# Kernel tuning notes

Hardware: AMD Instinct MI355X
Metric: run time of the kernel (lower is better)

The kernel has to match this reference:

```python
import jax, jax.numpy as jnp
import numpy as np

B, C, H, W = 2, 512, 48, 48
HEADS = 8
REDUCTION = 4
DPH = max(C // REDUCTION // HEADS, 1)   # 16
TOTAL = DPH * HEADS                      # 128
EPS_NORM = 1e-12
EPS_BN = 1e-5


def setup_inputs() -> dict:
    key = jax.random.key(0)
    ks = jax.random.split(key, 6)
    x = jax.random.normal(ks[0], (B, C, H, W), dtype=jnp.float32)
    # 1x1 convs stored as [out_ch, in_ch] matrices
    w_qkv = jax.random.normal(ks[1], (3 * TOTAL, C), dtype=jnp.float32) * (1.0 / np.sqrt(C))
    w_out = jax.random.normal(ks[2], (C, TOTAL), dtype=jnp.float32) * (1.0 / np.sqrt(TOTAL))
    temperature = jnp.ones((HEADS, 1, 1), dtype=jnp.float32)
    bn_gamma = jnp.ones((C,), dtype=jnp.float32)
    bn_beta = jnp.zeros((C,), dtype=jnp.float32)
    return {"x": x, "w_qkv": w_qkv, "temperature": temperature,
            "w_out": w_out, "bn_gamma": bn_gamma, "bn_beta": bn_beta}


def _l2norm(t):
    # F.normalize(t, dim=-1): t / max(||t||_2, eps)
    n = jnp.sqrt(jnp.sum(t * t, axis=-1, keepdims=True))
    return t / jnp.maximum(n, EPS_NORM)


def reference(x, w_qkv, temperature, w_out, bn_gamma, bn_beta):
    b, c, h, w = x.shape
    n = h * w
    # qkv 1x1 conv: [b, 3*TOTAL, h, w]
    qkv = jnp.einsum('bchw,oc->bohw', x, w_qkv)
    q, k, v = jnp.split(qkv, 3, axis=1)
    # [b, heads, dph, n] -> [b, heads, n, dph]
    def heads_tokens(t):
        return t.reshape(b, HEADS, DPH, n).transpose(0, 1, 3, 2)
    q = _l2norm(heads_tokens(q))
    k = _l2norm(heads_tokens(k))
    v = heads_tokens(v)
    # [b, heads, n, n]
    attn = jnp.einsum('bhnd,bhmd->bhnm', q, k) * temperature[None]
    attn = jax.nn.softmax(attn, axis=-1)
    out = jnp.einsum('bhnm,bhmd->bhnd', attn, v)          # [b, heads, n, dph]
    out = out.transpose(0, 1, 3, 2).reshape(b, TOTAL, h, w)
    # project_out: 1x1 conv then BatchNorm2d (training-mode batch stats)
    out = jnp.einsum('bthw,ct->bchw', out, w_out)
    mean = jnp.mean(out, axis=(0, 2, 3))
    var = jnp.mean((out - mean[None, :, None, None]) ** 2, axis=(0, 2, 3))
    out = (out - mean[None, :, None, None]) * jax.lax.rsqrt(var + EPS_BN)[None, :, None, None]
    out = out * bn_gamma[None, :, None, None] + bn_beta[None, :, None, None]
    return out
```

## Files before the change

kernel.cpp:

```cpp
#include <hip/hip_runtime.h>

#define NB 2
#define CC 512
#define NN 2304
#define NH 8
#define DD 16
#define TT 128
#define O3 384

typedef __attribute__((ext_vector_type(4))) float f32x4;
typedef __attribute__((ext_vector_type(8))) __bf16 bf16x8;
typedef __attribute__((ext_vector_type(4))) __bf16 bf16x4;
typedef __attribute__((ext_vector_type(4))) _Float16 f16x4;

__global__ __launch_bounds__(256) void k0_convert(
    const float* __restrict__ x, const float* __restrict__ wqkv,
    const float* __restrict__ wout,
    __bf16* __restrict__ xT, __bf16* __restrict__ wqb, __bf16* __restrict__ wob)
{
    int bid = blockIdx.x;
    int t = threadIdx.x;
    if (bid < 576) {
        __shared__ float tile[64][65];
        int b = bid / 288, rem = bid % 288;
        int nt = rem / 8, cb = rem % 8;
        int n0 = nt * 64, c0 = cb * 64;
        int tc = t >> 6, tn = t & 63;
#pragma unroll
        for (int i = 0; i < 16; i++) {
            int cl = i * 4 + tc;
            tile[cl][tn] = x[(size_t)(b * CC + c0 + cl) * NN + n0 + tn];
        }
        __syncthreads();
#pragma unroll
        for (int i = 0; i < 16; i++) {
            int nl = i * 4 + tc;
            xT[(size_t)(b * NN + n0 + nl) * CC + c0 + tn] = (__bf16)tile[tn][nl];
        }
    } else {
        int wid = bid - 576;
        int base = wid * 256 + t;
#pragma unroll
        for (int i = 0; i < 16; i++) {
            int j = base + i * 16384;
            if (j < O3 * CC) wqb[j] = (__bf16)wqkv[j];
            else             wob[j - O3 * CC] = (__bf16)wout[j - O3 * CC];
        }
    }
}

__global__ __launch_bounds__(256) void k1_qkv(
    const __bf16* __restrict__ xT, const __bf16* __restrict__ wqb,
    _Float16* __restrict__ Q, _Float16* __restrict__ K, _Float16* __restrict__ VT)
{
    int ob = blockIdx.x, nt = blockIdx.y, b = blockIdx.z;
    int lane = threadIdx.x & 63, wave = threadIdx.x >> 6;
    int quad = lane >> 4, col = lane & 15;
    int n0 = nt * 64 + wave * 16;
    int o0 = ob * 32;

    f32x4 acc[2];
    acc[0] = (f32x4){0.f, 0.f, 0.f, 0.f};
    acc[1] = (f32x4){0.f, 0.f, 0.f, 0.f};

    const __bf16* arow = xT + (size_t)(b * NN + n0 + col) * CC + quad * 8;
    const __bf16* brow0 = wqb + (size_t)(o0 + col) * CC + quad * 8;
    const __bf16* brow1 = brow0 + 16 * CC;

    bf16x8 a  = *(const bf16x8*)(arow);
    bf16x8 w0 = *(const bf16x8*)(brow0);
    bf16x8 w1 = *(const bf16x8*)(brow1);
#pragma unroll
    for (int ks = 0; ks < 16; ks++) {
        bf16x8 an, wn0, wn1;
        if (ks < 15) {
            an  = *(const bf16x8*)(arow + (ks + 1) * 32);
            wn0 = *(const bf16x8*)(brow0 + (ks + 1) * 32);
            wn1 = *(const bf16x8*)(brow1 + (ks + 1) * 32);
        }
        acc[0] = __builtin_amdgcn_mfma_f32_16x16x32_bf16(a, w0, acc[0], 0, 0, 0);
        acc[1] = __builtin_amdgcn_mfma_f32_16x16x32_bf16(a, w1, acc[1], 0, 0, 0);
        a = an; w0 = wn0; w1 = wn1;
    }

#pragma unroll
    for (int s = 0; s < 2; s++) {
        int oc = o0 + s * 16 + col;
        int d = oc & 15, h = (oc >> 4) & 7, kind = oc >> 7;
        f32x4 v = acc[s];
        if (kind < 2) {
            float ss0 = v[0] * v[0], ss1 = v[1] * v[1], ss2 = v[2] * v[2], ss3 = v[3] * v[3];
#pragma unroll
            for (int m = 1; m < 16; m <<= 1) {
                ss0 += __shfl_xor(ss0, m);
                ss1 += __shfl_xor(ss1, m);
                ss2 += __shfl_xor(ss2, m);
                ss3 += __shfl_xor(ss3, m);
            }
            v[0] *= 1.0f / fmaxf(sqrtf(ss0), 1e-12f);
            v[1] *= 1.0f / fmaxf(sqrtf(ss1), 1e-12f);
            v[2] *= 1.0f / fmaxf(sqrtf(ss2), 1e-12f);
            v[3] *= 1.0f / fmaxf(sqrtf(ss3), 1e-12f);
            _Float16* dst = (kind == 0 ? Q : K) + (size_t)(b * NH + h) * NN * DD;
#pragma unroll
            for (int r = 0; r < 4; r++) {
                int n = n0 + quad * 4 + r;
                dst[(size_t)n * DD + d] = (_Float16)v[r];
            }
        } else {
            f16x4 pk;
#pragma unroll
            for (int r = 0; r < 4; r++) pk[r] = (_Float16)v[r];
            int n = n0 + quad * 4;
            *(f16x4*)(VT + (size_t)((b * NH + h) * DD + d) * NN + n) = pk;
        }
    }
}

__global__ __launch_bounds__(256) void k2_attn(
    const _Float16* __restrict__ Q, const _Float16* __restrict__ K,
    const _Float16* __restrict__ VT, const float* __restrict__ temp,
    float* __restrict__ Opart, float* __restrict__ Lpart)
{
    int qt = blockIdx.x, bh = blockIdx.y, sp = blockIdx.z;
    int lane = threadIdx.x & 63, wave = threadIdx.x >> 6;
    int quad = lane >> 4, col = lane & 15;
    int kbase = sp * 288;
    int qbase = qt * 256 + wave * 64;

    const _Float16* Qb = Q + (size_t)bh * NN * DD;
    float tl2 = temp[bh & 7] * 1.4426950408889634f;

    f16x4 qf0 = *(const f16x4*)(Qb + (size_t)(qbase +  0 + col) * DD + quad * 4);
    f16x4 qf1 = *(const f16x4*)(Qb + (size_t)(qbase + 16 + col) * DD + quad * 4);
    f16x4 qf2 = *(const f16x4*)(Qb + (size_t)(qbase + 32 + col) * DD + quad * 4);
    f16x4 qf3 = *(const f16x4*)(Qb + (size_t)(qbase + 48 + col) * DD + quad * 4);

    f32x4 oa0 = {0.f,0.f,0.f,0.f}, oa1 = {0.f,0.f,0.f,0.f};
    f32x4 oa2 = {0.f,0.f,0.f,0.f}, oa3 = {0.f,0.f,0.f,0.f};
    float la0 = 0.f, la1 = 0.f, la2 = 0.f, la3 = 0.f;
    const f32x4 zc = {0.f,0.f,0.f,0.f};

    const _Float16* kp = K + (size_t)bh * NN * DD + (size_t)(kbase + col) * DD + quad * 4;
    const _Float16* vp = VT + (size_t)bh * DD * NN + (size_t)col * NN + kbase + quad * 4;

    f16x4 kfa = *(const f16x4*)(kp);
    f16x4 kfb = *(const f16x4*)(kp + 16 * DD);
    f16x4 vfa = *(const f16x4*)(vp);
    f16x4 vfb = *(const f16x4*)(vp + 16);

#define K2_CHUNK(KF, VF)                                                        \
    {                                                                           \
        f32x4 s0 = __builtin_amdgcn_mfma_f32_16x16x16f16(KF, qf0, zc, 0, 0, 0); \
        f32x4 s1 = __builtin_amdgcn_mfma_f32_16x16x16f16(KF, qf1, zc, 0, 0, 0); \
        f32x4 s2 = __builtin_amdgcn_mfma_f32_16x16x16f16(KF, qf2, zc, 0, 0, 0); \
        f32x4 s3 = __builtin_amdgcn_mfma_f32_16x16x16f16(KF, qf3, zc, 0, 0, 0); \
        f16x4 p0, p1, p2, p3;                                                   \
        _Pragma("unroll")                                                       \
        for (int r = 0; r < 4; ++r) {                                           \
            float e0 = __builtin_amdgcn_exp2f(tl2 * s0[r]);                     \
            float e1 = __builtin_amdgcn_exp2f(tl2 * s1[r]);                     \
            float e2 = __builtin_amdgcn_exp2f(tl2 * s2[r]);                     \
            float e3 = __builtin_amdgcn_exp2f(tl2 * s3[r]);                     \
            p0[r] = (_Float16)e0; la0 += e0;                                    \
            p1[r] = (_Float16)e1; la1 += e1;                                    \
            p2[r] = (_Float16)e2; la2 += e2;                                    \
            p3[r] = (_Float16)e3; la3 += e3;                                    \
        }                                                                       \
        oa0 = __builtin_amdgcn_mfma_f32_16x16x16f16(VF, p0, oa0, 0, 0, 0);      \
        oa1 = __builtin_amdgcn_mfma_f32_16x16x16f16(VF, p1, oa1, 0, 0, 0);      \
        oa2 = __builtin_amdgcn_mfma_f32_16x16x16f16(VF, p2, oa2, 0, 0, 0);      \
        oa3 = __builtin_amdgcn_mfma_f32_16x16x16f16(VF, p3, oa3, 0, 0, 0);      \
    }

    for (int g = 0; g < 9; ++g) {
        f16x4 kna, knb, vna, vnb;
        if (g < 8) {
            kna = *(const f16x4*)(kp + 32 * DD);
            knb = *(const f16x4*)(kp + 48 * DD);
            vna = *(const f16x4*)(vp + 32);
            vnb = *(const f16x4*)(vp + 48);
        }
        K2_CHUNK(kfa, vfa)
        K2_CHUNK(kfb, vfb)
        kfa = kna; kfb = knb; vfa = vna; vfb = vnb;
        kp += 32 * DD; vp += 32;
    }
#undef K2_CHUNK

    la0 += __shfl_xor(la0, 16); la0 += __shfl_xor(la0, 32);
    la1 += __shfl_xor(la1, 16); la1 += __shfl_xor(la1, 32);
    la2 += __shfl_xor(la2, 16); la2 += __shfl_xor(la2, 32);
    la3 += __shfl_xor(la3, 16); la3 += __shfl_xor(la3, 32);

    float* Ob = Opart + (((size_t)sp * 16 + bh) * DD + quad * 4) * NN + qbase + col;
#pragma unroll
    for (int r = 0; r < 4; ++r) {
        Ob[(size_t)r * NN +  0] = oa0[r];
        Ob[(size_t)r * NN + 16] = oa1[r];
        Ob[(size_t)r * NN + 32] = oa2[r];
        Ob[(size_t)r * NN + 48] = oa3[r];
    }
    float lv = (quad == 0) ? la0 : (quad == 1) ? la1 : (quad == 2) ? la2 : la3;
    Lpart[((size_t)sp * 16 + bh) * NN + qbase + quad * 16 + col] = lv;
}

__global__ __launch_bounds__(256) void k2c_combine(
    const float* __restrict__ Opart, const float* __restrict__ Lpart,
    __bf16* __restrict__ AO)
{
    int gid = blockIdx.x * 256 + threadIdx.x;
    int bh = gid / NN, n = gid % NN;
    int b = bh >> 3, h = bh & 7;
    float l = 0.f;
#pragma unroll
    for (int sp = 0; sp < 8; sp++)
        l += Lpart[((size_t)sp * 16 + bh) * NN + n];
    float inv = 1.0f / l;
    float o[16];
#pragma unroll
    for (int d = 0; d < 16; d++) o[d] = 0.f;
#pragma unroll
    for (int sp = 0; sp < 8; sp++) {
        const float* Ob = Opart + ((size_t)sp * 16 + bh) * DD * NN + n;
#pragma unroll
        for (int d = 0; d < 16; d++) o[d] += Ob[(size_t)d * NN];
    }
    bf16x8 v0, v1;
#pragma unroll
    for (int d = 0; d < 8; d++) v0[d] = (__bf16)(o[d] * inv);
#pragma unroll
    for (int d = 0; d < 8; d++) v1[d] = (__bf16)(o[d + 8] * inv);
    __bf16* dst = AO + (size_t)b * NN * TT + (size_t)n * TT + h * DD;
    *(bf16x8*)dst = v0;
    *(bf16x8*)(dst + 8) = v1;
}

__global__ __launch_bounds__(256) void k3_proj(
    const __bf16* __restrict__ AO, const __bf16* __restrict__ wob,
    float* __restrict__ out)
{
    int cb = blockIdx.x, nt = blockIdx.y, b = blockIdx.z;
    int lane = threadIdx.x & 63, wave = threadIdx.x >> 6;
    int quad = lane >> 4, col = lane & 15;
    int n0 = nt * 64 + wave * 16, c0 = cb * 32;

    f32x4 acc[2];
    acc[0] = (f32x4){0.f, 0.f, 0.f, 0.f};
    acc[1] = (f32x4){0.f, 0.f, 0.f, 0.f};

    const __bf16* ab = AO + (size_t)(b * NN + n0 + col) * TT + quad * 8;
    const __bf16* wb0 = wob + (size_t)(c0 + col) * TT + quad * 8;
    const __bf16* wb1 = wb0 + 16 * TT;
#pragma unroll
    for (int ks = 0; ks < 4; ks++) {
        bf16x8 a  = *(const bf16x8*)(ab + ks * 32);
        bf16x8 w0 = *(const bf16x8*)(wb0 + ks * 32);
        bf16x8 w1 = *(const bf16x8*)(wb1 + ks * 32);
        acc[0] = __builtin_amdgcn_mfma_f32_16x16x32_bf16(a, w0, acc[0], 0, 0, 0);
        acc[1] = __builtin_amdgcn_mfma_f32_16x16x32_bf16(a, w1, acc[1], 0, 0, 0);
    }
#pragma unroll
    for (int s = 0; s < 2; s++) {
        int c = c0 + s * 16 + col;
        float* dst = out + (size_t)(b * CC + c) * NN + n0 + quad * 4;
        *(f32x4*)dst = acc[s];
    }
}

__global__ __launch_bounds__(256) void k4_bn(
    float* __restrict__ out, const float* __restrict__ gamma,
    const float* __restrict__ beta)
{
    int c = blockIdx.x;
    int t = threadIdx.x;
    float vals[18];
    float s = 0.f, q = 0.f;
#pragma unroll
    for (int i = 0; i < 18; i++) {
        int j = i * 256 + t;
        int b = j / NN, n = j % NN;
        float v = out[(size_t)(b * CC + c) * NN + n];
        vals[i] = v; s += v; q += v * v;
    }
#pragma unroll
    for (int m = 1; m < 64; m <<= 1) { s += __shfl_xor(s, m); q += __shfl_xor(q, m); }
    __shared__ float rs[4], rq[4];
    int lane = t & 63, wave = t >> 6;
    if (lane == 0) { rs[wave] = s; rq[wave] = q; }
    __syncthreads();
    s = rs[0] + rs[1] + rs[2] + rs[3];
    q = rq[0] + rq[1] + rq[2] + rq[3];
    float mean = s * (1.0f / 4608.0f);
    float var = q * (1.0f / 4608.0f) - mean * mean;
    float sc = rsqrtf(var + 1e-5f) * gamma[c];
    float sh = beta[c] - mean * sc;
#pragma unroll
    for (int i = 0; i < 18; i++) {
        int j = i * 256 + t;
        int b = j / NN, n = j % NN;
        out[(size_t)(b * CC + c) * NN + n] = vals[i] * sc + sh;
    }
}

extern "C" void kernel_launch(void* const* d_in, const int* in_sizes, int n_in,
                              void* d_out, int out_size, void* d_ws, size_t ws_size,
                              hipStream_t stream) {
    const float* x     = (const float*)d_in[0];
    const float* wqkv  = (const float*)d_in[1];
    const float* temp  = (const float*)d_in[2];
    const float* wout  = (const float*)d_in[3];
    const float* gamma = (const float*)d_in[4];
    const float* beta  = (const float*)d_in[5];
    float* out = (float*)d_out;

    char* ws = (char*)d_ws;
    const size_t OFF_XT = 0;
    const size_t OFF_WQ = 4718592;
    const size_t OFF_WO = 5111808;
    const size_t OFF_Q  = 5242880;
    const size_t OFF_K  = 6422528;
    const size_t OFF_VT = 7602176;
    const size_t OFF_AO = 8781824;
    const size_t OFF_OP = 9961472;
    const size_t OFF_LP = 28835840;

    __bf16* xT  = (__bf16*)(ws + OFF_XT);
    __bf16* wqb = (__bf16*)(ws + OFF_WQ);
    __bf16* wob = (__bf16*)(ws + OFF_WO);
    _Float16* Q  = (_Float16*)(ws + OFF_Q);
    _Float16* K  = (_Float16*)(ws + OFF_K);
    _Float16* VT = (_Float16*)(ws + OFF_VT);
    __bf16* AO  = (__bf16*)(ws + OFF_AO);
    float* Opart = (float*)(ws + OFF_OP);
    float* Lpart = (float*)(ws + OFF_LP);

    k0_convert<<<640, 256, 0, stream>>>(x, wqkv, wout, xT, wqb, wob);
    k1_qkv<<<dim3(12, 36, 2), 256, 0, stream>>>(xT, wqb, Q, K, VT);
    k2_attn<<<dim3(9, 16, 8), 256, 0, stream>>>(Q, K, VT, temp, Opart, Lpart);
    k2c_combine<<<144, 256, 0, stream>>>(Opart, Lpart, AO);
    k3_proj<<<dim3(16, 36, 2), 256, 0, stream>>>(AO, wob, out);
    k4_bn<<<512, 256, 0, stream>>>(out, gamma, beta);
}
```

Baseline: 141.9 us.

## Fuse fp32-to-bf16 conversion and transpose into QKV and projection GEMMs

Removes the separate conversion kernel that transposed x to bf16 and converted the weights. The QKV GEMM now reads fp32 x directly in its native channel-major layout, swapping MFMA operand roles so tokens map to columns, and converts to bf16 on the fly. The L2-norm reduction becomes a cross-quad shuffle and the Q/K stores are vectorised. The projection converts the fp32 weights inline. This saves a launch and a full round trip of x through memory, at the cost of strided scalar fp32 loads of x inside the GEMM and repeated weight conversion across blocks.

Measured after the change: 149.2 us. +5.2%, slower.

```diff
diff --git a/kernel.cpp b/kernel.cpp
--- a/kernel.cpp
+++ b/kernel.cpp
@@ -10,47 +10,19 @@
 
 typedef __attribute__((ext_vector_type(4))) float f32x4;
 typedef __attribute__((ext_vector_type(8))) __bf16 bf16x8;
-typedef __attribute__((ext_vector_type(4))) __bf16 bf16x4;
 typedef __attribute__((ext_vector_type(4))) _Float16 f16x4;
 
-__global__ __launch_bounds__(256) void k0_convert(
+static __device__ __forceinline__ bf16x8 cvt8(const float* __restrict__ p) {
+    f32x4 lo = *(const f32x4*)p;
+    f32x4 hi = *(const f32x4*)(p + 4);
+    bf16x8 r;
+#pragma unroll
+    for (int i = 0; i < 4; i++) { r[i] = (__bf16)lo[i]; r[4 + i] = (__bf16)hi[i]; }
+    return r;
+}
+
+__global__ __launch_bounds__(256) void k1_qkv(
     const float* __restrict__ x, const float* __restrict__ wqkv,
-    const float* __restrict__ wout,
-    __bf16* __restrict__ xT, __bf16* __restrict__ wqb, __bf16* __restrict__ wob)
-{
-    int bid = blockIdx.x;
-    int t = threadIdx.x;
-    if (bid < 576) {
-        __shared__ float tile[64][65];
-        int b = bid / 288, rem = bid % 288;
-        int nt = rem / 8, cb = rem % 8;
-        int n0 = nt * 64, c0 = cb * 64;
-        int tc = t >> 6, tn = t & 63;
-#pragma unroll
-        for (int i = 0; i < 16; i++) {
-            int cl = i * 4 + tc;
-            tile[cl][tn] = x[(size_t)(b * CC + c0 + cl) * NN + n0 + tn];
-        }
-        __syncthreads();
-#pragma unroll
-        for (int i = 0; i < 16; i++) {
-            int nl = i * 4 + tc;
-            xT[(size_t)(b * NN + n0 + nl) * CC + c0 + tn] = (__bf16)tile[tn][nl];
-        }
-    } else {
-        int wid = bid - 576;
-        int base = wid * 256 + t;
-#pragma unroll
-        for (int i = 0; i < 16; i++) {
-            int j = base + i * 16384;
-            if (j < O3 * CC) wqb[j] = (__bf16)wqkv[j];
-            else             wob[j - O3 * CC] = (__bf16)wout[j - O3 * CC];
-        }
-    }
-}
-
-__global__ __launch_bounds__(256) void k1_qkv(
-    const __bf16* __restrict__ xT, const __bf16* __restrict__ wqb,
     _Float16* __restrict__ Q, _Float16* __restrict__ K, _Float16* __restrict__ VT)
 {
     int ob = blockIdx.x, nt = blockIdx.y, b = blockIdx.z;
@@ -59,60 +31,51 @@
     int n0 = nt * 64 + wave * 16;
     int o0 = ob * 32;
 
-    f32x4 acc[2];
-    acc[0] = (f32x4){0.f, 0.f, 0.f, 0.f};
-    acc[1] = (f32x4){0.f, 0.f, 0.f, 0.f};
-
-    const __bf16* arow = xT + (size_t)(b * NN + n0 + col) * CC + quad * 8;
-    const __bf16* brow0 = wqb + (size_t)(o0 + col) * CC + quad * 8;
-    const __bf16* brow1 = brow0 + 16 * CC;
-
-    bf16x8 a  = *(const bf16x8*)(arow);
-    bf16x8 w0 = *(const bf16x8*)(brow0);
-    bf16x8 w1 = *(const bf16x8*)(brow1);
-#pragma unroll
+    f32x4 acc0 = {0.f,0.f,0.f,0.f}, acc1 = {0.f,0.f,0.f,0.f};
+
+    const float* wr0 = wqkv + (size_t)(o0 + col) * CC + quad * 8;
+    const float* wr1 = wr0 + 16 * CC;
+    const float* xb  = x + (size_t)b * CC * NN + (size_t)(quad * 8) * NN + n0 + col;
+
+#pragma unroll 4
     for (int ks = 0; ks < 16; ks++) {
-        bf16x8 an, wn0, wn1;
-        if (ks < 15) {
-            an  = *(const bf16x8*)(arow + (ks + 1) * 32);
-            wn0 = *(const bf16x8*)(brow0 + (ks + 1) * 32);
-            wn1 = *(const bf16x8*)(brow1 + (ks + 1) * 32);
-        }
-        acc[0] = __builtin_amdgcn_mfma_f32_16x16x32_bf16(a, w0, acc[0], 0, 0, 0);
-        acc[1] = __builtin_amdgcn_mfma_f32_16x16x32_bf16(a, w1, acc[1], 0, 0, 0);
-        a = an; w0 = wn0; w1 = wn1;
-    }
-
+        const float* xc = xb + (size_t)(ks * 32) * NN;
+        bf16x8 bb;
+        bb[0] = (__bf16)xc[0];
+        bb[1] = (__bf16)xc[NN];
+        bb[2] = (__bf16)xc[2 * NN];
+        bb[3] = (__bf16)xc[3 * NN];
+        bb[4] = (__bf16)xc[4 * NN];
+        bb[5] = (__bf16)xc[5 * NN];
+        bb[6] = (__bf16)xc[6 * NN];
+        bb[7] = (__bf16)xc[7 * NN];
+        bf16x8 w0 = cvt8(wr0 + ks * 32);
+        bf16x8 w1 = cvt8(wr1 + ks * 32);
+        acc0 = __builtin_amdgcn_mfma_f32_16x16x32_bf16(w0, bb, acc0, 0, 0, 0);
+        acc1 = __builtin_amdgcn_mfma_f32_16x16x32_bf16(w1, bb, acc1, 0, 0, 0);
+    }
+
+    int kind = o0 >> 7;
 #pragma unroll
     for (int s = 0; s < 2; s++) {
-        int oc = o0 + s * 16 + col;
-        int d = oc & 15, h = (oc >> 4) & 7, kind = oc >> 7;
-        f32x4 v = acc[s];
+        f32x4 v = s ? acc1 : acc0;
+        int h = ((o0 + s * 16) >> 4) & 7;
+        int bh = b * NH + h;
         if (kind < 2) {
-            float ss0 = v[0] * v[0], ss1 = v[1] * v[1], ss2 = v[2] * v[2], ss3 = v[3] * v[3];
-#pragma unroll
-            for (int m = 1; m < 16; m <<= 1) {
-                ss0 += __shfl_xor(ss0, m);
-                ss1 += __shfl_xor(ss1, m);
-                ss2 += __shfl_xor(ss2, m);
-                ss3 += __shfl_xor(ss3, m);
-            }
-            v[0] *= 1.0f / fmaxf(sqrtf(ss0), 1e-12f);
-            v[1] *= 1.0f / fmaxf(sqrtf(ss1), 1e-12f);
-            v[2] *= 1.0f / fmaxf(sqrtf(ss2), 1e-12f);
-            v[3] *= 1.0f / fmaxf(sqrtf(ss3), 1e-12f);
-            _Float16* dst = (kind == 0 ? Q : K) + (size_t)(b * NH + h) * NN * DD;
-#pragma unroll
-            for (int r = 0; r < 4; r++) {
-                int n = n0 + quad * 4 + r;
-                dst[(size_t)n * DD + d] = (_Float16)v[r];
-            }
+            float ss = v[0]*v[0] + v[1]*v[1] + v[2]*v[2] + v[3]*v[3];
+            ss += __shfl_xor(ss, 16);
+            ss += __shfl_xor(ss, 32);
+            float inv = 1.0f / fmaxf(sqrtf(ss), 1e-12f);
+            f16x4 pk;
+#pragma unroll
+            for (int r = 0; r < 4; r++) pk[r] = (_Float16)(v[r] * inv);
+            _Float16* dst = (kind == 0 ? Q : K)
+                          + ((size_t)bh * NN + n0 + col) * DD + quad * 4;
+            *(f16x4*)dst = pk;
         } else {
-            f16x4 pk;
-#pragma unroll
-            for (int r = 0; r < 4; r++) pk[r] = (_Float16)v[r];
-            int n = n0 + quad * 4;
-            *(f16x4*)(VT + (size_t)((b * NH + h) * DD + d) * NN + n) = pk;
+#pragma unroll
+            for (int r = 0; r < 4; r++)
+                VT[((size_t)bh * DD + quad * 4 + r) * NN + n0 + col] = (_Float16)v[r];
         }
     }
 }
@@ -237,7 +200,7 @@
 }
 
 __global__ __launch_bounds__(256) void k3_proj(
-    const __bf16* __restrict__ AO, const __bf16* __restrict__ wob,
+    const __bf16* __restrict__ AO, const float* __restrict__ wout,
     float* __restrict__ out)
 {
     int cb = blockIdx.x, nt = blockIdx.y, b = blockIdx.z;
@@ -245,26 +208,24 @@
     int quad = lane >> 4, col = lane & 15;
     int n0 = nt * 64 + wave * 16, c0 = cb * 32;
 
-    f32x4 acc[2];
-    acc[0] = (f32x4){0.f, 0.f, 0.f, 0.f};
-    acc[1] = (f32x4){0.f, 0.f, 0.f, 0.f};
+    f32x4 acc0 = {0.f,0.f,0.f,0.f}, acc1 = {0.f,0.f,0.f,0.f};
 
     const __bf16* ab = AO + (size_t)(b * NN + n0 + col) * TT + quad * 8;
-    const __bf16* wb0 = wob + (size_t)(c0 + col) * TT + quad * 8;
-    const __bf16* wb1 = wb0 + 16 * TT;
+    const float* wb0 = wout + (size_t)(c0 + col) * TT + quad * 8;
+    const float* wb1 = wb0 + 16 * TT;
 #pragma unroll
     for (int ks = 0; ks < 4; ks++) {
         bf16x8 a  = *(const bf16x8*)(ab + ks * 32);
-        bf16x8 w0 = *(const bf16x8*)(wb0 + ks * 32);
-        bf16x8 w1 = *(const bf16x8*)(wb1 + ks * 32);
-        acc[0] = __builtin_amdgcn_mfma_f32_16x16x32_bf16(a, w0, acc[0], 0, 0, 0);
-        acc[1] = __builtin_amdgcn_mfma_f32_16x16x32_bf16(a, w1, acc[1], 0, 0, 0);
+        bf16x8 w0 = cvt8(wb0 + ks * 32);
+        bf16x8 w1 = cvt8(wb1 + ks * 32);
+        acc0 = __builtin_amdgcn_mfma_f32_16x16x32_bf16(a, w0, acc0, 0, 0, 0);
+        acc1 = __builtin_amdgcn_mfma_f32_16x16x32_bf16(a, w1, acc1, 0, 0, 0);
     }
 #pragma unroll
     for (int s = 0; s < 2; s++) {
         int c = c0 + s * 16 + col;
         float* dst = out + (size_t)(b * CC + c) * NN + n0 + quad * 4;
-        *(f32x4*)dst = acc[s];
+        *(f32x4*)dst = s ? acc1 : acc0;
     }
 }
 
@@ -315,30 +276,23 @@
     float* out = (float*)d_out;
 
     char* ws = (char*)d_ws;
-    const size_t OFF_XT = 0;
-    const size_t OFF_WQ = 4718592;
-    const size_t OFF_WO = 5111808;
-    const size_t OFF_Q  = 5242880;
-    const size_t OFF_K  = 6422528;
-    const size_t OFF_VT = 7602176;
-    const size_t OFF_AO = 8781824;
-    const size_t OFF_OP = 9961472;
-    const size_t OFF_LP = 28835840;
-
-    __bf16* xT  = (__bf16*)(ws + OFF_XT);
-    __bf16* wqb = (__bf16*)(ws + OFF_WQ);
-    __bf16* wob = (__bf16*)(ws + OFF_WO);
+    const size_t OFF_Q  = 0;
+    const size_t OFF_K  = 1179648;
+    const size_t OFF_VT = 2359296;
+    const size_t OFF_AO = 3538944;
+    const size_t OFF_OP = 4718592;
+    const size_t OFF_LP = 23592960;
+
     _Float16* Q  = (_Float16*)(ws + OFF_Q);
     _Float16* K  = (_Float16*)(ws + OFF_K);
     _Float16* VT = (_Float16*)(ws + OFF_VT);
-    __bf16* AO  = (__bf16*)(ws + OFF_AO);
+    __bf16* AO   = (__bf16*)(ws + OFF_AO);
     float* Opart = (float*)(ws + OFF_OP);
     float* Lpart = (float*)(ws + OFF_LP);
 
-    k0_convert<<<640, 256, 0, stream>>>(x, wqkv, wout, xT, wqb, wob);
-    k1_qkv<<<dim3(12, 36, 2), 256, 0, stream>>>(xT, wqb, Q, K, VT);
+    k1_qkv<<<dim3(12, 36, 2), 256, 0, stream>>>(x, wqkv, Q, K, VT);
     k2_attn<<<dim3(9, 16, 8), 256, 0, stream>>>(Q, K, VT, temp, Opart, Lpart);
     k2c_combine<<<144, 256, 0, stream>>>(Opart, Lpart, AO);
-    k3_proj<<<dim3(16, 36, 2), 256, 0, stream>>>(AO, wob, out);
+    k3_proj<<<dim3(16, 36, 2), 256, 0, stream>>>(AO, wout, out);
     k4_bn<<<512, 256, 0, stream>>>(out, gamma, beta);
 }
```

## Store attention partials as bf16 token-major and sum row via MFMA

Applied to the files above, without the earlier changes.

The split-K attention partial outputs become bf16 instead of fp32, and their layout changes from d-major to token-major. This halves the partial-buffer traffic between the attention and combine kernels and lets combine use vector loads. The softmax denominator is now accumulated with an extra MFMA against a ones vector instead of scalar adds and cross-lane shuffles. The fp32-to-fp16 conversions now use packed round-toward-zero. Costs are extra MFMA issue per chunk and lower precision in the stored partial sums.

Result: no change. 142.6 us (+0.6%).

```diff
diff --git a/kernel.cpp b/kernel.cpp
--- a/kernel.cpp
+++ b/kernel.cpp
@@ -59,11 +59,8 @@
     int n0 = nt * 64 + wave * 16;
     int o0 = ob * 32;
 
-    f32x4 acc[2];
-    acc[0] = (f32x4){0.f, 0.f, 0.f, 0.f};
-    acc[1] = (f32x4){0.f, 0.f, 0.f, 0.f};
-
-    const __bf16* arow = xT + (size_t)(b * NN + n0 + col) * CC + quad * 8;
+    f32x4 acc0 = {0.f,0.f,0.f,0.f}, acc1 = {0.f,0.f,0.f,0.f};
+    const __bf16* arow  = xT + (size_t)(b * NN + n0 + col) * CC + quad * 8;
     const __bf16* brow0 = wqb + (size_t)(o0 + col) * CC + quad * 8;
     const __bf16* brow1 = brow0 + 16 * CC;
 
@@ -78,18 +75,18 @@
             wn0 = *(const bf16x8*)(brow0 + (ks + 1) * 32);
             wn1 = *(const bf16x8*)(brow1 + (ks + 1) * 32);
         }
-        acc[0] = __builtin_amdgcn_mfma_f32_16x16x32_bf16(a, w0, acc[0], 0, 0, 0);
-        acc[1] = __builtin_amdgcn_mfma_f32_16x16x32_bf16(a, w1, acc[1], 0, 0, 0);
+        acc0 = __builtin_amdgcn_mfma_f32_16x16x32_bf16(a, w0, acc0, 0, 0, 0);
+        acc1 = __builtin_amdgcn_mfma_f32_16x16x32_bf16(a, w1, acc1, 0, 0, 0);
         a = an; w0 = wn0; w1 = wn1;
     }
 
 #pragma unroll
     for (int s = 0; s < 2; s++) {
+        f32x4 v = s ? acc1 : acc0;
         int oc = o0 + s * 16 + col;
         int d = oc & 15, h = (oc >> 4) & 7, kind = oc >> 7;
-        f32x4 v = acc[s];
         if (kind < 2) {
-            float ss0 = v[0] * v[0], ss1 = v[1] * v[1], ss2 = v[2] * v[2], ss3 = v[3] * v[3];
+            float ss0 = v[0]*v[0], ss1 = v[1]*v[1], ss2 = v[2]*v[2], ss3 = v[3]*v[3];
 #pragma unroll
             for (int m = 1; m < 16; m <<= 1) {
                 ss0 += __shfl_xor(ss0, m);
@@ -103,16 +100,13 @@
             v[3] *= 1.0f / fmaxf(sqrtf(ss3), 1e-12f);
             _Float16* dst = (kind == 0 ? Q : K) + (size_t)(b * NH + h) * NN * DD;
 #pragma unroll
-            for (int r = 0; r < 4; r++) {
-                int n = n0 + quad * 4 + r;
-                dst[(size_t)n * DD + d] = (_Float16)v[r];
-            }
+            for (int r = 0; r < 4; r++)
+                dst[(size_t)(n0 + quad * 4 + r) * DD + d] = (_Float16)v[r];
         } else {
             f16x4 pk;
 #pragma unroll
             for (int r = 0; r < 4; r++) pk[r] = (_Float16)v[r];
-            int n = n0 + quad * 4;
-            *(f16x4*)(VT + (size_t)((b * NH + h) * DD + d) * NN + n) = pk;
+            *(f16x4*)(VT + (size_t)((b * NH + h) * DD + d) * NN + n0 + quad * 4) = pk;
         }
     }
 }
@@ -120,7 +114,7 @@
 __global__ __launch_bounds__(256) void k2_attn(
     const _Float16* __restrict__ Q, const _Float16* __restrict__ K,
     const _Float16* __restrict__ VT, const float* __restrict__ temp,
-    float* __restrict__ Opart, float* __restrict__ Lpart)
+    __bf16* __restrict__ Opart, float* __restrict__ Lpart)
 {
     int qt = blockIdx.x, bh = blockIdx.y, sp = blockIdx.z;
     int lane = threadIdx.x & 63, wave = threadIdx.x >> 6;
@@ -138,8 +132,12 @@
 
     f32x4 oa0 = {0.f,0.f,0.f,0.f}, oa1 = {0.f,0.f,0.f,0.f};
     f32x4 oa2 = {0.f,0.f,0.f,0.f}, oa3 = {0.f,0.f,0.f,0.f};
-    float la0 = 0.f, la1 = 0.f, la2 = 0.f, la3 = 0.f;
+    f32x4 la0 = {0.f,0.f,0.f,0.f}, la1 = {0.f,0.f,0.f,0.f};
+    f32x4 la2 = {0.f,0.f,0.f,0.f}, la3 = {0.f,0.f,0.f,0.f};
     const f32x4 zc = {0.f,0.f,0.f,0.f};
+    f16x4 onef;
+#pragma unroll
+    for (int i = 0; i < 4; i++) onef[i] = (_Float16)1.0f;
 
     const _Float16* kp = K + (size_t)bh * NN * DD + (size_t)(kbase + col) * DD + quad * 4;
     const _Float16* vp = VT + (size_t)bh * DD * NN + (size_t)col * NN + kbase + quad * 4;
@@ -148,6 +146,18 @@
     f16x4 kfb = *(const f16x4*)(kp + 16 * DD);
     f16x4 vfa = *(const f16x4*)(vp);
     f16x4 vfb = *(const f16x4*)(vp + 16);
+
+#define K2_EXPP(SF, PF)                                                         \
+    {                                                                           \
+        float e0 = __builtin_amdgcn_exp2f(tl2 * SF[0]);                         \
+        float e1 = __builtin_amdgcn_exp2f(tl2 * SF[1]);                         \
+        float e2 = __builtin_amdgcn_exp2f(tl2 * SF[2]);                         \
+        float e3 = __builtin_amdgcn_exp2f(tl2 * SF[3]);                         \
+        auto lo = __builtin_amdgcn_cvt_pkrtz(e0, e1);                           \
+        auto hi = __builtin_amdgcn_cvt_pkrtz(e2, e3);                           \
+        PF[0] = (_Float16)lo[0]; PF[1] = (_Float16)lo[1];                       \
+        PF[2] = (_Float16)hi[0]; PF[3] = (_Float16)hi[1];                       \
+    }
 
 #define K2_CHUNK(KF, VF)                                                        \
     {                                                                           \
@@ -156,21 +166,15 @@
         f32x4 s2 = __builtin_amdgcn_mfma_f32_16x16x16f16(KF, qf2, zc, 0, 0, 0); \
         f32x4 s3 = __builtin_amdgcn_mfma_f32_16x16x16f16(KF, qf3, zc, 0, 0, 0); \
         f16x4 p0, p1, p2, p3;                                                   \
-        _Pragma("unroll")                                                       \
-        for (int r = 0; r < 4; ++r) {                                           \
-            float e0 = __builtin_amdgcn_exp2f(tl2 * s0[r]);                     \
-            float e1 = __builtin_amdgcn_exp2f(tl2 * s1[r]);                     \
-            float e2 = __builtin_amdgcn_exp2f(tl2 * s2[r]);                     \
-            float e3 = __builtin_amdgcn_exp2f(tl2 * s3[r]);                     \
-            p0[r] = (_Float16)e0; la0 += e0;                                    \
-            p1[r] = (_Float16)e1; la1 += e1;                                    \
-            p2[r] = (_Float16)e2; la2 += e2;                                    \
-            p3[r] = (_Float16)e3; la3 += e3;                                    \
-        }                                                                       \
+        K2_EXPP(s0, p0) K2_EXPP(s1, p1) K2_EXPP(s2, p2) K2_EXPP(s3, p3)         \
         oa0 = __builtin_amdgcn_mfma_f32_16x16x16f16(VF, p0, oa0, 0, 0, 0);      \
         oa1 = __builtin_amdgcn_mfma_f32_16x16x16f16(VF, p1, oa1, 0, 0, 0);      \
         oa2 = __builtin_amdgcn_mfma_f32_16x16x16f16(VF, p2, oa2, 0, 0, 0);      \
         oa3 = __builtin_amdgcn_mfma_f32_16x16x16f16(VF, p3, oa3, 0, 0, 0);      \
+        la0 = __builtin_amdgcn_mfma_f32_16x16x16f16(onef, p0, la0, 0, 0, 0);    \
+        la1 = __builtin_amdgcn_mfma_f32_16x16x16f16(onef, p1, la1, 0, 0, 0);    \
+        la2 = __builtin_amdgcn_mfma_f32_16x16x16f16(onef, p2, la2, 0, 0, 0);    \
+        la3 = __builtin_amdgcn_mfma_f32_16x16x16f16(onef, p3, la3, 0, 0, 0);    \
     }
 
     for (int g = 0; g < 9; ++g) {
@@ -187,26 +191,26 @@
         kp += 32 * DD; vp += 32;
     }
 #undef K2_CHUNK
-
-    la0 += __shfl_xor(la0, 16); la0 += __shfl_xor(la0, 32);
-    la1 += __shfl_xor(la1, 16); la1 += __shfl_xor(la1, 32);
-    la2 += __shfl_xor(la2, 16); la2 += __shfl_xor(la2, 32);
-    la3 += __shfl_xor(la3, 16); la3 += __shfl_xor(la3, 32);
-
-    float* Ob = Opart + (((size_t)sp * 16 + bh) * DD + quad * 4) * NN + qbase + col;
+#undef K2_EXPP
+
+    __bf16* Ob = Opart + (((size_t)sp * 16 + bh) * NN + qbase) * DD + (size_t)col * DD + quad * 4;
+    bf16x4 w0, w1, w2, w3;
 #pragma unroll
     for (int r = 0; r < 4; ++r) {
-        Ob[(size_t)r * NN +  0] = oa0[r];
-        Ob[(size_t)r * NN + 16] = oa1[r];
-        Ob[(size_t)r * NN + 32] = oa2[r];
-        Ob[(size_t)r * NN + 48] = oa3[r];
-    }
-    float lv = (quad == 0) ? la0 : (quad == 1) ? la1 : (quad == 2) ? la2 : la3;
+        w0[r] = (__bf16)oa0[r]; w1[r] = (__bf16)oa1[r];
+        w2[r] = (__bf16)oa2[r]; w3[r] = (__bf16)oa3[r];
+    }
+    *(bf16x4*)(Ob)               = w0;
+    *(bf16x4*)(Ob + 16 * DD)     = w1;
+    *(bf16x4*)(Ob + 32 * DD)     = w2;
+    *(bf16x4*)(Ob + 48 * DD)     = w3;
+
+    float lv = (quad == 0) ? la0[0] : (quad == 1) ? la1[0] : (quad == 2) ? la2[0] : la3[0];
     Lpart[((size_t)sp * 16 + bh) * NN + qbase + quad * 16 + col] = lv;
 }
 
 __global__ __launch_bounds__(256) void k2c_combine(
-    const float* __restrict__ Opart, const float* __restrict__ Lpart,
+    const __bf16* __restrict__ Opart, const float* __restrict__ Lpart,
     __bf16* __restrict__ AO)
 {
     int gid = blockIdx.x * 256 + threadIdx.x;
@@ -222,9 +226,11 @@
     for (int d = 0; d < 16; d++) o[d] = 0.f;
 #pragma unroll
     for (int sp = 0; sp < 8; sp++) {
-        const float* Ob = Opart + ((size_t)sp * 16 + bh) * DD * NN + n;
-#pragma unroll
-        for (int d = 0; d < 16; d++) o[d] += Ob[(size_t)d * NN];
+        const __bf16* Ob = Opart + (((size_t)sp * 16 + bh) * NN + n) * DD;
+        bf16x8 lo = *(const bf16x8*)(Ob);
+        bf16x8 hi = *(const bf16x8*)(Ob + 8);
+#pragma unroll
+        for (int d = 0; d < 8; d++) { o[d] += (float)lo[d]; o[d + 8] += (float)hi[d]; }
     }
     bf16x8 v0, v1;
 #pragma unroll
@@ -245,11 +251,8 @@
     int quad = lane >> 4, col = lane & 15;
     int n0 = nt * 64 + wave * 16, c0 = cb * 32;
 
-    f32x4 acc[2];
-    acc[0] = (f32x4){0.f, 0.f, 0.f, 0.f};
-    acc[1] = (f32x4){0.f, 0.f, 0.f, 0.f};
-
-    const __bf16* ab = AO + (size_t)(b * NN + n0 + col) * TT + quad * 8;
+    f32x4 acc0 = {0.f,0.f,0.f,0.f}, acc1 = {0.f,0.f,0.f,0.f};
+    const __bf16* ab  = AO + (size_t)(b * NN + n0 + col) * TT + quad * 8;
     const __bf16* wb0 = wob + (size_t)(c0 + col) * TT + quad * 8;
     const __bf16* wb1 = wb0 + 16 * TT;
 #pragma unroll
@@ -257,14 +260,14 @@
         bf16x8 a  = *(const bf16x8*)(ab + ks * 32);
         bf16x8 w0 = *(const bf16x8*)(wb0 + ks * 32);
         bf16x8 w1 = *(const bf16x8*)(wb1 + ks * 32);
-        acc[0] = __builtin_amdgcn_mfma_f32_16x16x32_bf16(a, w0, acc[0], 0, 0, 0);
-        acc[1] = __builtin_amdgcn_mfma_f32_16x16x32_bf16(a, w1, acc[1], 0, 0, 0);
+        acc0 = __builtin_amdgcn_mfma_f32_16x16x32_bf16(a, w0, acc0, 0, 0, 0);
+        acc1 = __builtin_amdgcn_mfma_f32_16x16x32_bf16(a, w1, acc1, 0, 0, 0);
     }
 #pragma unroll
     for (int s = 0; s < 2; s++) {
         int c = c0 + s * 16 + col;
         float* dst = out + (size_t)(b * CC + c) * NN + n0 + quad * 4;
-        *(f32x4*)dst = acc[s];
+        *(f32x4*)dst = s ? acc1 : acc0;
     }
 }
 
@@ -323,7 +326,7 @@
     const size_t OFF_VT = 7602176;
     const size_t OFF_AO = 8781824;
     const size_t OFF_OP = 9961472;
-    const size_t OFF_LP = 28835840;
+    const size_t OFF_LP = 19398656;
 
     __bf16* xT  = (__bf16*)(ws + OFF_XT);
     __bf16* wqb = (__bf16*)(ws + OFF_WQ);
@@ -331,9 +334,9 @@
     _Float16* Q  = (_Float16*)(ws + OFF_Q);
     _Float16* K  = (_Float16*)(ws + OFF_K);
     _Float16* VT = (_Float16*)(ws + OFF_VT);
-    __bf16* AO  = (__bf16*)(ws + OFF_AO);
-    float* Opart = (float*)(ws + OFF_OP);
-    float* Lpart = (float*)(ws + OFF_LP);
+    __bf16* AO   = (__bf16*)(ws + OFF_AO);
+    __bf16* Opart = (__bf16*)(ws + OFF_OP);
+    float* Lpart  = (float*)(ws + OFF_LP);
 
     k0_convert<<<640, 256, 0, stream>>>(x, wqkv, wout, xT, wqb, wob);
     k1_qkv<<<dim3(12, 36, 2), 256, 0, stream>>>(xT, wqb, Q, K, VT);
```
